# Kernel tuning notes

Hardware: AMD Instinct MI355X
Metric: run time of the kernel (lower is better)

## Reference

```python
import jax, jax.numpy as jnp
import numpy as np

NUM_LEAVES = 8192
N_LAMBDA = 2101  # wavelengths 400..2500 nm

# ---- exponential integral E1(x), x > 0 (Abramowitz & Stegun 5.1.53 / 5.1.56) ----
# Ei(-x) = -E1(x) for x > 0; forward only ever calls expi on -kall with kall >= 1e-4.
_A = jnp.array([-0.57721566, 0.99999193, -0.24991055, 0.05519968, -0.00976004, 0.00107857], dtype=jnp.float32)
_PN = jnp.array([1.0, 8.5733287401, 18.0590169730, 8.6347608925, 0.2677737343], dtype=jnp.float32)
_PD = jnp.array([1.0, 9.5733223454, 25.6329561486, 21.0996530827, 3.9584969228], dtype=jnp.float32)

def _poly(c, x):
    r = c[0]
    for ci in c[1:]:
        r = r * x + ci
    return r

def _e1(x):
    # x > 0 guaranteed (kall clamped to >= 1e-4)
    small = -jnp.log(x) + _poly(_A[::-1], x)          # 0 < x <= 1
    big = jnp.exp(-x) / x * (_poly(_PN, x) / _poly(_PD, x))  # x > 1
    return jnp.where(x <= 1.0, small, big)

# ---- transmissivity of a dielectric plane (Stern / Allen) ----
def _getav(alpha_deg, nr):
    n2 = nr ** 2
    npx = n2 + 1.0
    nm = n2 - 1.0
    a = (nr + 1.0) * (nr + 1.0) / 2.0
    k = -(n2 - 1.0) * (n2 - 1.0) / 4.0
    rd = alpha_deg * (np.pi / 180.0)
    sa2 = np.sin(rd) ** 2  # python scalar
    if alpha_deg != 90.0:
        b1 = jnp.sqrt((sa2 - npx / 2.0) ** 2 + k)
    else:
        b1 = 0.0
    b2 = sa2 - npx / 2.0
    b = b1 - b2
    k2 = k ** 2
    ts = k2 / (6.0 * b ** 3) + k / b - b / 2.0 - (k2 / (6.0 * a ** 3) + k / a - a / 2.0)
    tp1 = -2.0 * n2 * (b - a) / npx ** 2
    nm2 = nm ** 2
    tp2 = -2.0 * n2 * npx * jnp.log(b / a) / nm2
    tp3 = n2 * (1.0 / b - 1.0 / a) / 2.0
    n22 = n2 ** 2
    npx3 = npx ** 3
    npax_a = 2.0 * npx * a - nm2
    npx_b = 2.0 * npx * b - nm2
    tp4 = 16.0 * n22 * (n22 + 1.0) * jnp.log(npx_b / npax_a) / (npx3 * nm2)
    tp5 = 16.0 * n2 ** 3 * (1.0 / npx_b - 1.0 / npax_a) / npx3
    tp = tp1 + tp2 + tp3 + tp4 + tp5
    return (ts + tp) / (2.0 * sa2)

def _forward(N, cab, car, water, lma, cant, nr, kab, kcar, kant, kw, km):
    # kall: [L, W] via broadcasting of [L,1] traits against [W] spectra
    kall = (cab * kab + car * kcar + cant * kant + water * kw + lma * km) / N
    kall = jnp.maximum(kall, 1e-4)
    # tau = (1-k)e^{-k} + k^2 * (-Ei(-k)) = (1-k)e^{-k} + k^2 E1(k)
    tau = (1.0 - kall) * jnp.exp(-kall) + kall ** 2 * _e1(kall)

    # one-layer reflectance/transmittance
    talf = _getav(40.0, nr)
    ralf = 1.0 - talf
    t12 = _getav(90.0, nr)
    r12 = 1.0 - t12
    t21 = t12 / (nr * nr)
    r21 = 1.0 - t21
    denom = 1.0 - r21 * r21 * tau * tau
    Ta = talf * tau * t21 / denom
    Ra = ralf + r21 * tau * Ta
    t = t12 * tau * t21 / denom
    r = r12 + r21 * tau * t

    rpt = r + t
    rmt = r - t
    mask = rpt >= 1.0  # [L, W]
    Dsq = (1.0 + rpt) * (1.0 + rmt) * (1.0 - rmt) * (1.0 - rpt)
    D = jnp.sqrt(jnp.where(mask, 1.0, Dsq))
    rqmtq = r ** 2 - t ** 2
    a = (1.0 + rqmtq + D) / (2.0 * r)
    b = (1.0 - rqmtq + D) / (2.0 * t)
    b_safe = jnp.where(mask, 1.0, b)  # guard pow with float exponent
    bnm1 = b_safe ** (N - 1.0)
    bn2 = bnm1 ** 2
    a2 = a * a
    den2 = a2 * bn2 - 1.0
    Rsub = a * (bn2 - 1.0) / den2
    Tsub = bnm1 * (a2 - 1.0) / den2
    # thick-layer (r+t >= 1) limit
    Tsub_alt = t / (t + (1.0 - t) * (N - 1.0))
    Tsub = jnp.where(mask, Tsub_alt, Tsub)
    Rsub = jnp.where(mask, 1.0 - Tsub_alt, Rsub)

    den3 = 1.0 - Rsub * r
    tran = Ta * Tsub / den3
    refl = Ra + Ta_Rsub_term(Ta, Rsub, t, den3)
    return refl, tran

def Ta_Rsub_term(Ta, Rsub, t, den3):
    return Ta * Rsub * t / den3

def setup_inputs() -> dict:
    key = jax.random.key(0)
    ks = jax.random.split(key, 12)
    u = lambda k, shp: jax.random.uniform(k, shp, dtype=jnp.float32)
    L, W = NUM_LEAVES, N_LAMBDA
    return {
        "N":     1.0 + 1.5 * u(ks[0], (L, 1)),      # leaf structure 1..2.5
        "cab":   10.0 + 70.0 * u(ks[1], (L, 1)),    # chlorophyll ug/cm2
        "car":   2.0 + 18.0 * u(ks[2], (L, 1)),     # carotenoids
        "water": 0.002 + 0.03 * u(ks[3], (L, 1)),   # EWT cm
        "lma":   0.005 + 0.03 * u(ks[4], (L, 1)),   # dry matter g/cm2
        "cant":  2.0 * u(ks[5], (L, 1)),            # anthocyanins
        "nr":    1.3 + 0.3 * u(ks[6], (W,)),        # refractive index
        "kab":   0.05 * u(ks[7], (W,)),
        "kcar":  0.05 * u(ks[8], (W,)),
        "kant":  0.05 * u(ks[9], (W,)),
        "kw":    30.0 * u(ks[10], (W,)),
        "km":    60.0 * u(ks[11], (W,)),
    }

def reference(N, cab, car, water, lma, cant, nr, kab, kcar, kant, kw, km):
    return _forward(N, cab, car, water, lma, cant, nr, kab, kcar, kant, kw, km)
```

## Files before the change

kernel.cpp:

```cpp
#include <hip/hip_runtime.h>
#include <hip/hip_fp16.h>

#define L_LEAVES 8192
#define W_LAMBDA 2101
#define WPAD     2104
#define TAB_N    1153
#define SA2_40   0.41317591116653485f
#define LOG2E_F  1.4426950408889634f
#define LN2_F    0.6931471805599453f

typedef float v2f __attribute__((ext_vector_type(2)));

__device__ __forceinline__ float rcpf(float x)  { return __builtin_amdgcn_rcpf(x); }
__device__ __forceinline__ float log2f_fast(float x) { return __builtin_amdgcn_logf(x); }
__device__ __forceinline__ float exp2f_fast(float x) { return __builtin_amdgcn_exp2f(x); }
__device__ __forceinline__ float sqrtf_fast(float x) { return __builtin_amdgcn_sqrtf(x); }
__device__ __forceinline__ v2f v2(float a, float b) { v2f r; r.x = a; r.y = b; return r; }

__device__ __forceinline__ float getav_dev(float sa2, bool is90, float nr) {
    float n2  = nr * nr;
    float npx = n2 + 1.0f;
    float nm  = n2 - 1.0f;
    float a   = (nr + 1.0f) * (nr + 1.0f) * 0.5f;
    float k   = -(n2 - 1.0f) * (n2 - 1.0f) * 0.25f;
    float b2  = sa2 - npx * 0.5f;
    float b1  = is90 ? 0.0f : sqrtf_fast(b2 * b2 + k);
    float b   = b1 - b2;
    float k2  = k * k;
    float ib  = rcpf(b), ia = rcpf(a);
    float ts  = k2 * (1.0f/6.0f) * (ib*ib*ib) + k * ib - b * 0.5f
              - (k2 * (1.0f/6.0f) * (ia*ia*ia) + k * ia - a * 0.5f);
    float inpx = rcpf(npx);
    float tp1 = -2.0f * n2 * (b - a) * (inpx * inpx);
    float nm2 = nm * nm;
    float inm2 = rcpf(nm2);
    float tp2 = -2.0f * n2 * npx * (LN2_F * log2f_fast(b * ia)) * inm2;
    float tp3 = n2 * (ib - ia) * 0.5f;
    float n22 = n2 * n2;
    float inpx3 = inpx * inpx * inpx;
    float npax_a = 2.0f * npx * a - nm2;
    float npx_b  = 2.0f * npx * b - nm2;
    float tp4 = 16.0f * n22 * (n22 + 1.0f) * (LN2_F * log2f_fast(npx_b * rcpf(npax_a))) * inpx3 * inm2;
    float tp5 = 16.0f * n2 * n2 * n2 * (rcpf(npx_b) - rcpf(npax_a)) * inpx3;
    float tp  = tp1 + tp2 + tp3 + tp4 + tp5;
    return (ts + tp) * rcpf(2.0f * sa2);
}

__device__ __forceinline__ float tau_exact(float k) {
    float ek = exp2f_fast(-k * LOG2E_F);
    float e1;
    if (k <= 1.0f) {
        float poly = fmaf(fmaf(fmaf(fmaf(fmaf(0.00107857f, k, -0.00976004f), k, 0.05519968f),
                        k, -0.24991055f), k, 0.99999193f), k, -0.57721566f);
        e1 = fmaf(-LN2_F, log2f_fast(k), poly);
    } else {
        float pn = fmaf(fmaf(fmaf(k + 8.5733287401f, k, 18.0590169730f),
                       k, 8.6347608925f), k, 0.2677737343f);
        float pd = fmaf(fmaf(fmaf(k + 9.5733223454f, k, 25.6329561486f),
                       k, 21.0996530827f), k, 3.9584969228f);
        e1 = ek * rcpf(k) * (pn * rcpf(pd));
    }
    return fmaf(k * k, e1, (1.0f - k) * ek);
}

__device__ __forceinline__ float bin_k(int w) {
    unsigned e = (unsigned)w >> 6, m = (unsigned)w & 63u;
    return __uint_as_float(((113u + e) << 23) | (m << 17));
}

__global__ void precompute_kernel(const float* __restrict__ nr, float* __restrict__ tab) {
    int w = blockIdx.x * blockDim.x + threadIdx.x;
    if (w < WPAD) {
        int ws = min(w, W_LAMBDA - 1);
        float n    = nr[ws];
        float talf = getav_dev(SA2_40, false, n);
        float t12  = getav_dev(1.0f,   true,  n);
        float t21  = t12 * rcpf(n * n);
        float r21  = 1.0f - t21;
        tab[0 * WPAD + w] = talf * t21;
        tab[1 * WPAD + w] = 1.0f - talf;
        tab[2 * WPAD + w] = t12 * t21;
        tab[3 * WPAD + w] = 1.0f - t12;
        tab[4 * WPAD + w] = r21;
    }
    if (w < TAB_N) {
        float T0 = tau_exact(bin_k(w));
        float T1 = tau_exact(bin_k(w + 1));
        __half2 h2;
        h2.x = __float2half(T0);
        h2.y = __float2half(T1 - T0);
        tab[5 * WPAD + w] = __uint_as_float(*reinterpret_cast<unsigned*>(&h2));
    }
}

struct f4u { float v[4]; };

template<bool USE_TAB>
__global__ __launch_bounds__(192) void prospect_kernel(
    const float* __restrict__ pN,   const float* __restrict__ pcab,
    const float* __restrict__ pcar, const float* __restrict__ pwater,
    const float* __restrict__ plma, const float* __restrict__ pcant,
    const float* __restrict__ pnr,
    const float* __restrict__ pkab, const float* __restrict__ pkcar,
    const float* __restrict__ pkant, const float* __restrict__ pkw,
    const float* __restrict__ pkm,
    const float* __restrict__ tab,
    float* __restrict__ out_r, float* __restrict__ out_t)
{
    __shared__ unsigned TT[TAB_N];
    if (USE_TAB) {
        const float* src = tab + 5 * WPAD;
        for (int i = threadIdx.x; i < TAB_N; i += 192)
            TT[i] = __float_as_uint(src[i]);
        __syncthreads();
    }

    const int q  = blockIdx.x * 192 + threadIdx.x;
    const int w0 = q * 4;
    if (w0 >= W_LAMBDA) return;
    const bool full = (w0 + 4 <= W_LAMBDA);

    const int l = blockIdx.y;
    const float Nl   = pN[l];
    const float invN = rcpf(Nl);
    const float Nm1  = Nl - 1.0f;
    const float cabl = pcab[l], carl = pcar[l], cantl = pcant[l];
    const float watl = pwater[l], lmal = plma[l];

    float4 vkab, vkcar, vkant, vkw, vkm;
    if (full) {
        vkab  = *(const float4*)(pkab  + w0);
        vkcar = *(const float4*)(pkcar + w0);
        vkant = *(const float4*)(pkant + w0);
        vkw   = *(const float4*)(pkw   + w0);
        vkm   = *(const float4*)(pkm   + w0);
    } else {
        #pragma unroll
        for (int j = 0; j < 4; ++j) {
            int w = min(w0 + j, W_LAMBDA - 1);
            ((float*)&vkab)[j]  = pkab[w];
            ((float*)&vkcar)[j] = pkcar[w];
            ((float*)&vkant)[j] = pkant[w];
            ((float*)&vkw)[j]   = pkw[w];
            ((float*)&vkm)[j]   = pkm[w];
        }
    }
    float4 t0, t1, t2, t3, t4;
    if (USE_TAB) {
        t0 = *(const float4*)(tab + 0 * WPAD + w0);
        t1 = *(const float4*)(tab + 1 * WPAD + w0);
        t2 = *(const float4*)(tab + 2 * WPAD + w0);
        t3 = *(const float4*)(tab + 3 * WPAD + w0);
        t4 = *(const float4*)(tab + 4 * WPAD + w0);
    } else {
        #pragma unroll
        for (int j = 0; j < 4; ++j) {
            int w = min(w0 + j, W_LAMBDA - 1);
            float n    = pnr[w];
            float talf = getav_dev(SA2_40, false, n);
            float t12  = getav_dev(1.0f,   true,  n);
            float t21  = t12 * rcpf(n * n);
            float r21  = 1.0f - t21;
            ((float*)&t0)[j] = talf * t21;
            ((float*)&t1)[j] = 1.0f - talf;
            ((float*)&t2)[j] = t12 * t21;
            ((float*)&t3)[j] = 1.0f - t12;
            ((float*)&t4)[j] = r21;
        }
    }

    float rf[4], tr[4];
    #pragma unroll
    for (int p = 0; p < 2; ++p) {
        const v2f c0 = p ? v2(t0.z, t0.w) : v2(t0.x, t0.y);
        const v2f c1 = p ? v2(t1.z, t1.w) : v2(t1.x, t1.y);
        const v2f c2 = p ? v2(t2.z, t2.w) : v2(t2.x, t2.y);
        const v2f c3 = p ? v2(t3.z, t3.w) : v2(t3.x, t3.y);
        const v2f c4 = p ? v2(t4.z, t4.w) : v2(t4.x, t4.y);
        const v2f ab = p ? v2(vkab.z, vkab.w) : v2(vkab.x, vkab.y);
        const v2f cr = p ? v2(vkcar.z, vkcar.w) : v2(vkcar.x, vkcar.y);
        const v2f an = p ? v2(vkant.z, vkant.w) : v2(vkant.x, vkant.y);
        const v2f wt = p ? v2(vkw.z, vkw.w) : v2(vkw.x, vkw.y);
        const v2f lm = p ? v2(vkm.z, vkm.w) : v2(vkm.x, vkm.y);

        v2f k = (cabl * ab + carl * cr + cantl * an + watl * wt + lmal * lm) * invN;
        k = __builtin_elementwise_max(k, (v2f)1e-4f);

        v2f tau;
        if (USE_TAB) {
            v2f kc = __builtin_elementwise_min(k, (v2f)15.9f);
            unsigned b0 = __float_as_uint(kc.x), b1 = __float_as_uint(kc.y);
            unsigned u0 = TT[(int)(b0 >> 17) - 7232];
            unsigned u1 = TT[(int)(b1 >> 17) - 7232];
            float2 Tf0 = __half22float2(*reinterpret_cast<const __half2*>(&u0));
            float2 Tf1 = __half22float2(*reinterpret_cast<const __half2*>(&u1));
            v2f frac = v2((float)(b0 & 0x1FFFFu), (float)(b1 & 0x1FFFFu)) * (1.0f / 131072.0f);
            tau = frac * v2(Tf0.y, Tf1.y) + v2(Tf0.x, Tf1.x);
        } else {
            tau = v2(tau_exact(k.x), tau_exact(k.y));
        }

        v2f r21t = c4 * tau;
        v2f d1   = 1.0f - r21t * r21t;
        v2f rd   = v2(rcpf(d1.x), rcpf(d1.y));
        v2f trd  = tau * rd;
        v2f Ta   = c0 * trd;
        v2f tt   = c2 * trd;
        v2f Ra   = r21t * Ta + c1;
        v2f rr   = r21t * tt + c3;

        v2f rpt = rr + tt;
        v2f rmt = rr - tt;
        bool m0 = (rpt.x >= 1.0f), m1 = (rpt.y >= 1.0f);
        v2f Dsq = (1.0f - rmt * rmt) * (1.0f - rpt * rpt);
        v2f D   = v2(sqrtf_fast(m0 ? 1.0f : Dsq.x), sqrtf_fast(m1 ? 1.0f : Dsq.y));
        v2f rq  = rpt * rmt;
        v2f s1  = 1.0f + D;
        v2f prod = (rr * tt) * 4.0f;
        v2f rp2  = v2(rcpf(prod.x), rcpf(prod.y));
        v2f aa   = (s1 + rq) * (rp2 * (tt + tt));
        v2f bb   = (s1 - rq) * (rp2 * (rr + rr));
        v2f lg   = v2(log2f_fast(m0 ? 1.0f : bb.x), log2f_fast(m1 ? 1.0f : bb.y));
        v2f ex   = Nm1 * lg;
        v2f bnm1 = v2(exp2f_fast(ex.x), exp2f_fast(ex.y));
        v2f bn2  = bnm1 * bnm1;
        v2f a2   = aa * aa;
        v2f den2 = a2 * bn2 - 1.0f;
        v2f bn2m1 = bn2 - 1.0f;
        v2f M    = den2 - (aa * rr) * bn2m1;
        v2f invM = v2(rcpf(M.x), rcpf(M.y));
        v2f TaM  = Ta * invM;
        v2f tranv = TaM * bnm1 * (a2 - 1.0f);
        v2f reflv = (TaM * tt * aa) * bn2m1 + Ra;

        if (__any((int)(m0 || m1))) {
            #pragma unroll
            for (int c = 0; c < 2; ++c) {
                bool m = c ? m1 : m0;
                if (m) {
                    float ttc = c ? tt.y : tt.x, rrc = c ? rr.y : rr.x;
                    float Tac = c ? Ta.y : Ta.x, Rac = c ? Ra.y : Ra.x;
                    float Talt = ttc * rcpf(fmaf(Nm1, 1.0f - ttc, ttc));
                    float Rsm  = 1.0f - Talt;
                    float g    = Tac * rcpf(fmaf(-Rsm, rrc, 1.0f));
                    if (c) { tranv.y = g * Talt; reflv.y = fmaf(g * Rsm, ttc, Rac); }
                    else   { tranv.x = g * Talt; reflv.x = fmaf(g * Rsm, ttc, Rac); }
                }
            }
        }

        tr[2 * p]     = tranv.x;
        tr[2 * p + 1] = tranv.y;
        rf[2 * p]     = reflv.x;
        rf[2 * p + 1] = reflv.y;
    }

    const unsigned base = (unsigned)l * W_LAMBDA + (unsigned)w0;
    if (full) {
        f4u fr; f4u ft;
        #pragma unroll
        for (int j = 0; j < 4; ++j) { fr.v[j] = rf[j]; ft.v[j] = tr[j]; }
        *reinterpret_cast<f4u*>(out_r + base) = fr;
        *reinterpret_cast<f4u*>(out_t + base) = ft;
    } else {
        out_r[base] = rf[0];
        out_t[base] = tr[0];
    }
}

extern "C" void kernel_launch(void* const* d_in, const int* in_sizes, int n_in,
                              void* d_out, int out_size, void* d_ws, size_t ws_size,
                              hipStream_t stream) {
    const float* pN     = (const float*)d_in[0];
    const float* pcab   = (const float*)d_in[1];
    const float* pcar   = (const float*)d_in[2];
    const float* pwater = (const float*)d_in[3];
    const float* plma   = (const float*)d_in[4];
    const float* pcant  = (const float*)d_in[5];
    const float* pnr    = (const float*)d_in[6];
    const float* pkab   = (const float*)d_in[7];
    const float* pkcar  = (const float*)d_in[8];
    const float* pkant  = (const float*)d_in[9];
    const float* pkw    = (const float*)d_in[10];
    const float* pkm    = (const float*)d_in[11];
    float* out_r = (float*)d_out;
    float* out_t = out_r + (size_t)L_LEAVES * W_LAMBDA;

    const int nquads = (W_LAMBDA + 3) / 4;
    dim3 grid((nquads + 191) / 192, L_LEAVES);
    dim3 block(192);

    const size_t tab_bytes = (5 * WPAD + TAB_N) * sizeof(float);
    if (ws_size >= tab_bytes) {
        float* tabp = (float*)d_ws;
        precompute_kernel<<<(WPAD + 63) / 64, 64, 0, stream>>>(pnr, tabp);
        prospect_kernel<true><<<grid, block, 0, stream>>>(
            pN, pcab, pcar, pwater, plma, pcant, pnr,
            pkab, pkcar, pkant, pkw, pkm, (const float*)tabp, out_r, out_t);
    } else {
        prospect_kernel<false><<<grid, block, 0, stream>>>(
            pN, pcab, pcar, pwater, plma, pcant, pnr,
            pkab, pkcar, pkant, pkw, pkm, nullptr, out_r, out_t);
    }
}
```

Baseline: 52.82 us.

## Use one 576-thread block per leaf with scalar tail threads

Measured after the change: 51.27 us (median of 2 runs). 1.03x faster.

```diff
diff --git a/kernel.cpp b/kernel.cpp
--- a/kernel.cpp
+++ b/kernel.cpp
@@ -93,10 +93,49 @@
     }
 }
 
+__device__ __forceinline__ void stokes_point(float tau, float c0, float c1, float c2,
+                                             float c3, float c4, float Nm1,
+                                             float& refl, float& tran) {
+    float r21t = c4 * tau;
+    float rd   = rcpf(fmaf(-r21t, r21t, 1.0f));
+    float trd  = tau * rd;
+    float Ta   = c0 * trd;
+    float tt   = c2 * trd;
+    float Ra   = fmaf(r21t, Ta, c1);
+    float rr   = fmaf(r21t, tt, c3);
+    float rpt  = rr + tt;
+    float rmt  = rr - tt;
+    bool  mask = (rpt >= 1.0f);
+    float Dsq  = fmaf(-rmt, rmt, 1.0f) * fmaf(-rpt, rpt, 1.0f);
+    float D    = sqrtf_fast(mask ? 1.0f : Dsq);
+    float rq   = rpt * rmt;
+    float s1   = 1.0f + D;
+    float rp2  = rcpf((rr * tt) * 4.0f);
+    float aa   = (s1 + rq) * (rp2 * (tt + tt));
+    float bb   = (s1 - rq) * (rp2 * (rr + rr));
+    float bnm1 = exp2f_fast(Nm1 * log2f_fast(mask ? 1.0f : bb));
+    float bn2  = bnm1 * bnm1;
+    float a2   = aa * aa;
+    float den2 = fmaf(a2, bn2, -1.0f);
+    float bn2m1 = bn2 - 1.0f;
+    float M    = fmaf(-aa * rr, bn2m1, den2);
+    float invM = rcpf(M);
+    float TaM  = Ta * invM;
+    tran = TaM * bnm1 * (a2 - 1.0f);
+    refl = fmaf(TaM * tt * aa, bn2m1, Ra);
+    if (mask) {
+        float Talt = tt * rcpf(fmaf(Nm1, 1.0f - tt, tt));
+        float Rsm  = 1.0f - Talt;
+        float g    = Ta * rcpf(fmaf(-Rsm, rr, 1.0f));
+        tran = g * Talt;
+        refl = fmaf(g * Rsm, tt, Ra);
+    }
+}
+
 struct f4u { float v[4]; };
 
 template<bool USE_TAB>
-__global__ __launch_bounds__(192) void prospect_kernel(
+__global__ __launch_bounds__(576) void prospect_kernel(
     const float* __restrict__ pN,   const float* __restrict__ pcab,
     const float* __restrict__ pcar, const float* __restrict__ pwater,
     const float* __restrict__ plma, const float* __restrict__ pcant,
@@ -110,161 +149,186 @@
     __shared__ unsigned TT[TAB_N];
     if (USE_TAB) {
         const float* src = tab + 5 * WPAD;
-        for (int i = threadIdx.x; i < TAB_N; i += 192)
+        for (int i = threadIdx.x; i < TAB_N; i += 576)
             TT[i] = __float_as_uint(src[i]);
         __syncthreads();
     }
 
-    const int q  = blockIdx.x * 192 + threadIdx.x;
-    const int w0 = q * 4;
-    if (w0 >= W_LAMBDA) return;
-    const bool full = (w0 + 4 <= W_LAMBDA);
-
-    const int l = blockIdx.y;
+    const int l = blockIdx.x;
     const float Nl   = pN[l];
     const float invN = rcpf(Nl);
     const float Nm1  = Nl - 1.0f;
     const float cabl = pcab[l], carl = pcar[l], cantl = pcant[l];
     const float watl = pwater[l], lmal = plma[l];
-
-    float4 vkab, vkcar, vkant, vkw, vkm;
-    if (full) {
-        vkab  = *(const float4*)(pkab  + w0);
-        vkcar = *(const float4*)(pkcar + w0);
-        vkant = *(const float4*)(pkant + w0);
-        vkw   = *(const float4*)(pkw   + w0);
-        vkm   = *(const float4*)(pkm   + w0);
-    } else {
+    const int tid = threadIdx.x;
+    const unsigned rowbase = (unsigned)l * W_LAMBDA;
+
+    if (tid < 512) {
+        const int w0 = tid * 4;
+
+        float4 vkab  = *(const float4*)(pkab  + w0);
+        float4 vkcar = *(const float4*)(pkcar + w0);
+        float4 vkant = *(const float4*)(pkant + w0);
+        float4 vkw   = *(const float4*)(pkw   + w0);
+        float4 vkm   = *(const float4*)(pkm   + w0);
+        float4 t0, t1, t2, t3, t4;
+        if (USE_TAB) {
+            t0 = *(const float4*)(tab + 0 * WPAD + w0);
+            t1 = *(const float4*)(tab + 1 * WPAD + w0);
+            t2 = *(const float4*)(tab + 2 * WPAD + w0);
+            t3 = *(const float4*)(tab + 3 * WPAD + w0);
+            t4 = *(const float4*)(tab + 4 * WPAD + w0);
+        } else {
+            #pragma unroll
+            for (int j = 0; j < 4; ++j) {
+                int w = w0 + j;
+                float n    = pnr[w];
+                float talf = getav_dev(SA2_40, false, n);
+                float t12  = getav_dev(1.0f,   true,  n);
+                float t21  = t12 * rcpf(n * n);
+                float r21  = 1.0f - t21;
+                ((float*)&t0)[j] = talf * t21;
+                ((float*)&t1)[j] = 1.0f - talf;
+                ((float*)&t2)[j] = t12 * t21;
+                ((float*)&t3)[j] = 1.0f - t12;
+                ((float*)&t4)[j] = r21;
+            }
+        }
+
+        float rf[4], tr[4];
         #pragma unroll
-        for (int j = 0; j < 4; ++j) {
-            int w = min(w0 + j, W_LAMBDA - 1);
-            ((float*)&vkab)[j]  = pkab[w];
-            ((float*)&vkcar)[j] = pkcar[w];
-            ((float*)&vkant)[j] = pkant[w];
-            ((float*)&vkw)[j]   = pkw[w];
-            ((float*)&vkm)[j]   = pkm[w];
+        for (int p = 0; p < 2; ++p) {
+            const v2f c0 = p ? v2(t0.z, t0.w) : v2(t0.x, t0.y);
+            const v2f c1 = p ? v2(t1.z, t1.w) : v2(t1.x, t1.y);
+            const v2f c2 = p ? v2(t2.z, t2.w) : v2(t2.x, t2.y);
+            const v2f c3 = p ? v2(t3.z, t3.w) : v2(t3.x, t3.y);
+            const v2f c4 = p ? v2(t4.z, t4.w) : v2(t4.x, t4.y);
+            const v2f ab = p ? v2(vkab.z, vkab.w) : v2(vkab.x, vkab.y);
+            const v2f cr = p ? v2(vkcar.z, vkcar.w) : v2(vkcar.x, vkcar.y);
+            const v2f an = p ? v2(vkant.z, vkant.w) : v2(vkant.x, vkant.y);
+            const v2f wt = p ? v2(vkw.z, vkw.w) : v2(vkw.x, vkw.y);
+            const v2f lm = p ? v2(vkm.z, vkm.w) : v2(vkm.x, vkm.y);
+
+            v2f k = (cabl * ab + carl * cr + cantl * an + watl * wt + lmal * lm) * invN;
+            k = __builtin_elementwise_max(k, (v2f)1e-4f);
+
+            v2f tau;
+            if (USE_TAB) {
+                v2f kc = __builtin_elementwise_min(k, (v2f)15.9f);
+                unsigned b0 = __float_as_uint(kc.x), b1 = __float_as_uint(kc.y);
+                unsigned u0 = TT[(int)(b0 >> 17) - 7232];
+                unsigned u1 = TT[(int)(b1 >> 17) - 7232];
+                float2 Tf0 = __half22float2(*reinterpret_cast<const __half2*>(&u0));
+                float2 Tf1 = __half22float2(*reinterpret_cast<const __half2*>(&u1));
+                v2f frac = v2((float)(b0 & 0x1FFFFu), (float)(b1 & 0x1FFFFu)) * (1.0f / 131072.0f);
+                tau = frac * v2(Tf0.y, Tf1.y) + v2(Tf0.x, Tf1.x);
+            } else {
+                tau = v2(tau_exact(k.x), tau_exact(k.y));
+            }
+
+            v2f r21t = c4 * tau;
+            v2f d1   = 1.0f - r21t * r21t;
+            v2f rd   = v2(rcpf(d1.x), rcpf(d1.y));
+            v2f trd  = tau * rd;
+            v2f Ta   = c0 * trd;
+            v2f tt   = c2 * trd;
+            v2f Ra   = r21t * Ta + c1;
+            v2f rr   = r21t * tt + c3;
+
+            v2f rpt = rr + tt;
+            v2f rmt = rr - tt;
+            bool m0 = (rpt.x >= 1.0f), m1 = (rpt.y >= 1.0f);
+            v2f Dsq = (1.0f - rmt * rmt) * (1.0f - rpt * rpt);
+            v2f D   = v2(sqrtf_fast(m0 ? 1.0f : Dsq.x), sqrtf_fast(m1 ? 1.0f : Dsq.y));
+            v2f rq  = rpt * rmt;
+            v2f s1  = 1.0f + D;
+            v2f prod = (rr * tt) * 4.0f;
+            v2f rp2  = v2(rcpf(prod.x), rcpf(prod.y));
+            v2f aa   = (s1 + rq) * (rp2 * (tt + tt));
+            v2f bb   = (s1 - rq) * (rp2 * (rr + rr));
+            v2f lg   = v2(log2f_fast(m0 ? 1.0f : bb.x), log2f_fast(m1 ? 1.0f : bb.y));
+            v2f ex   = Nm1 * lg;
+            v2f bnm1 = v2(exp2f_fast(ex.x), exp2f_fast(ex.y));
+            v2f bn2  = bnm1 * bnm1;
+            v2f a2   = aa * aa;
+            v2f den2 = a2 * bn2 - 1.0f;
+            v2f bn2m1 = bn2 - 1.0f;
+            v2f M    = den2 - (aa * rr) * bn2m1;
+            v2f invM = v2(rcpf(M.x), rcpf(M.y));
+            v2f TaM  = Ta * invM;
+            v2f tranv = TaM * bnm1 * (a2 - 1.0f);
+            v2f reflv = (TaM * tt * aa) * bn2m1 + Ra;
+
+            if (__any((int)(m0 || m1))) {
+                #pragma unroll
+                for (int c = 0; c < 2; ++c) {
+                    bool m = c ? m1 : m0;
+                    if (m) {
+                        float ttc = c ? tt.y : tt.x, rrc = c ? rr.y : rr.x;
+                        float Tac = c ? Ta.y : Ta.x, Rac = c ? Ra.y : Ra.x;
+                        float Talt = ttc * rcpf(fmaf(Nm1, 1.0f - ttc, ttc));
+                        float Rsm  = 1.0f - Talt;
+                        float g    = Tac * rcpf(fmaf(-Rsm, rrc, 1.0f));
+                        if (c) { tranv.y = g * Talt; reflv.y = fmaf(g * Rsm, ttc, Rac); }
+                        else   { tranv.x = g * Talt; reflv.x = fmaf(g * Rsm, ttc, Rac); }
+                    }
+                }
+            }
+
+            tr[2 * p]     = tranv.x;
+            tr[2 * p + 1] = tranv.y;
+            rf[2 * p]     = reflv.x;
+            rf[2 * p + 1] = reflv.y;
         }
-    }
-    float4 t0, t1, t2, t3, t4;
-    if (USE_TAB) {
-        t0 = *(const float4*)(tab + 0 * WPAD + w0);
-        t1 = *(const float4*)(tab + 1 * WPAD + w0);
-        t2 = *(const float4*)(tab + 2 * WPAD + w0);
-        t3 = *(const float4*)(tab + 3 * WPAD + w0);
-        t4 = *(const float4*)(tab + 4 * WPAD + w0);
-    } else {
-        #pragma unroll
-        for (int j = 0; j < 4; ++j) {
-            int w = min(w0 + j, W_LAMBDA - 1);
-            float n    = pnr[w];
-            float talf = getav_dev(SA2_40, false, n);
-            float t12  = getav_dev(1.0f,   true,  n);
-            float t21  = t12 * rcpf(n * n);
-            float r21  = 1.0f - t21;
-            ((float*)&t0)[j] = talf * t21;
-            ((float*)&t1)[j] = 1.0f - talf;
-            ((float*)&t2)[j] = t12 * t21;
-            ((float*)&t3)[j] = 1.0f - t12;
-            ((float*)&t4)[j] = r21;
-        }
-    }
-
-    float rf[4], tr[4];
-    #pragma unroll
-    for (int p = 0; p < 2; ++p) {
-        const v2f c0 = p ? v2(t0.z, t0.w) : v2(t0.x, t0.y);
-        const v2f c1 = p ? v2(t1.z, t1.w) : v2(t1.x, t1.y);
-        const v2f c2 = p ? v2(t2.z, t2.w) : v2(t2.x, t2.y);
-        const v2f c3 = p ? v2(t3.z, t3.w) : v2(t3.x, t3.y);
-        const v2f c4 = p ? v2(t4.z, t4.w) : v2(t4.x, t4.y);
-        const v2f ab = p ? v2(vkab.z, vkab.w) : v2(vkab.x, vkab.y);
-        const v2f cr = p ? v2(vkcar.z, vkcar.w) : v2(vkcar.x, vkcar.y);
-        const v2f an = p ? v2(vkant.z, vkant.w) : v2(vkant.x, vkant.y);
-        const v2f wt = p ? v2(vkw.z, vkw.w) : v2(vkw.x, vkw.y);
-        const v2f lm = p ? v2(vkm.z, vkm.w) : v2(vkm.x, vkm.y);
-
-        v2f k = (cabl * ab + carl * cr + cantl * an + watl * wt + lmal * lm) * invN;
-        k = __builtin_elementwise_max(k, (v2f)1e-4f);
-
-        v2f tau;
-        if (USE_TAB) {
-            v2f kc = __builtin_elementwise_min(k, (v2f)15.9f);
-            unsigned b0 = __float_as_uint(kc.x), b1 = __float_as_uint(kc.y);
-            unsigned u0 = TT[(int)(b0 >> 17) - 7232];
-            unsigned u1 = TT[(int)(b1 >> 17) - 7232];
-            float2 Tf0 = __half22float2(*reinterpret_cast<const __half2*>(&u0));
-            float2 Tf1 = __half22float2(*reinterpret_cast<const __half2*>(&u1));
-            v2f frac = v2((float)(b0 & 0x1FFFFu), (float)(b1 & 0x1FFFFu)) * (1.0f / 131072.0f);
-            tau = frac * v2(Tf0.y, Tf1.y) + v2(Tf0.x, Tf1.x);
-        } else {
-            tau = v2(tau_exact(k.x), tau_exact(k.y));
-        }
-
-        v2f r21t = c4 * tau;
-        v2f d1   = 1.0f - r21t * r21t;
-        v2f rd   = v2(rcpf(d1.x), rcpf(d1.y));
-        v2f trd  = tau * rd;
-        v2f Ta   = c0 * trd;
-        v2f tt   = c2 * trd;
-        v2f Ra   = r21t * Ta + c1;
-        v2f rr   = r21t * tt + c3;
-
-        v2f rpt = rr + tt;
-        v2f rmt = rr - tt;
-        bool m0 = (rpt.x >= 1.0f), m1 = (rpt.y >= 1.0f);
-        v2f Dsq = (1.0f - rmt * rmt) * (1.0f - rpt * rpt);
-        v2f D   = v2(sqrtf_fast(m0 ? 1.0f : Dsq.x), sqrtf_fast(m1 ? 1.0f : Dsq.y));
-        v2f rq  = rpt * rmt;
-        v2f s1  = 1.0f + D;
-        v2f prod = (rr * tt) * 4.0f;
-        v2f rp2  = v2(rcpf(prod.x), rcpf(prod.y));
-        v2f aa   = (s1 + rq) * (rp2 * (tt + tt));
-        v2f bb   = (s1 - rq) * (rp2 * (rr + rr));
-        v2f lg   = v2(log2f_fast(m0 ? 1.0f : bb.x), log2f_fast(m1 ? 1.0f : bb.y));
-        v2f ex   = Nm1 * lg;
-        v2f bnm1 = v2(exp2f_fast(ex.x), exp2f_fast(ex.y));
-        v2f bn2  = bnm1 * bnm1;
-        v2f a2   = aa * aa;
-        v2f den2 = a2 * bn2 - 1.0f;
-        v2f bn2m1 = bn2 - 1.0f;
-        v2f M    = den2 - (aa * rr) * bn2m1;
-        v2f invM = v2(rcpf(M.x), rcpf(M.y));
-        v2f TaM  = Ta * invM;
-        v2f tranv = TaM * bnm1 * (a2 - 1.0f);
-        v2f reflv = (TaM * tt * aa) * bn2m1 + Ra;
-
-        if (__any((int)(m0 || m1))) {
-            #pragma unroll
-            for (int c = 0; c < 2; ++c) {
-                bool m = c ? m1 : m0;
-                if (m) {
-                    float ttc = c ? tt.y : tt.x, rrc = c ? rr.y : rr.x;
-                    float Tac = c ? Ta.y : Ta.x, Rac = c ? Ra.y : Ra.x;
-                    float Talt = ttc * rcpf(fmaf(Nm1, 1.0f - ttc, ttc));
-                    float Rsm  = 1.0f - Talt;
-                    float g    = Tac * rcpf(fmaf(-Rsm, rrc, 1.0f));
-                    if (c) { tranv.y = g * Talt; reflv.y = fmaf(g * Rsm, ttc, Rac); }
-                    else   { tranv.x = g * Talt; reflv.x = fmaf(g * Rsm, ttc, Rac); }
-                }
-            }
-        }
-
-        tr[2 * p]     = tranv.x;
-        tr[2 * p + 1] = tranv.y;
-        rf[2 * p]     = reflv.x;
-        rf[2 * p + 1] = reflv.y;
-    }
-
-    const unsigned base = (unsigned)l * W_LAMBDA + (unsigned)w0;
-    if (full) {
+
+        const unsigned base = rowbase + (unsigned)w0;
         f4u fr; f4u ft;
         #pragma unroll
         for (int j = 0; j < 4; ++j) { fr.v[j] = rf[j]; ft.v[j] = tr[j]; }
         *reinterpret_cast<f4u*>(out_r + base) = fr;
         *reinterpret_cast<f4u*>(out_t + base) = ft;
     } else {
-        out_r[base] = rf[0];
-        out_t[base] = tr[0];
+        const int w = 2048 + (tid - 512);
+        if (w < W_LAMBDA) {
+            float k = (cabl * pkab[w] + carl * pkcar[w] + cantl * pkant[w]
+                     + watl * pkw[w] + lmal * pkm[w]) * invN;
+            k = fmaxf(k, 1e-4f);
+
+            float c0, c1, c2, c3, c4;
+            if (USE_TAB) {
+                c0 = tab[0 * WPAD + w];
+                c1 = tab[1 * WPAD + w];
+                c2 = tab[2 * WPAD + w];
+                c3 = tab[3 * WPAD + w];
+                c4 = tab[4 * WPAD + w];
+            } else {
+                float n    = pnr[w];
+                float talf = getav_dev(SA2_40, false, n);
+                float t12  = getav_dev(1.0f,   true,  n);
+                float t21  = t12 * rcpf(n * n);
+                float r21  = 1.0f - t21;
+                c0 = talf * t21; c1 = 1.0f - talf; c2 = t12 * t21;
+                c3 = 1.0f - t12; c4 = r21;
+            }
+
+            float tau;
+            if (USE_TAB) {
+                float kc = fminf(k, 15.9f);
+                unsigned bits = __float_as_uint(kc);
+                int idx = (int)(bits >> 17) - 7232;
+                float frac = (float)(bits & 0x1FFFFu) * (1.0f / 131072.0f);
+                unsigned u = TT[idx];
+                float2 Tf = __half22float2(*reinterpret_cast<const __half2*>(&u));
+                tau = fmaf(frac, Tf.y, Tf.x);
+            } else {
+                tau = tau_exact(k);
+            }
+
+            float refl, tran;
+            stokes_point(tau, c0, c1, c2, c3, c4, Nm1, refl, tran);
+            out_r[rowbase + w] = refl;
+            out_t[rowbase + w] = tran;
+        }
     }
 }
 
@@ -286,9 +350,8 @@
     float* out_r = (float*)d_out;
     float* out_t = out_r + (size_t)L_LEAVES * W_LAMBDA;
 
-    const int nquads = (W_LAMBDA + 3) / 4;
-    dim3 grid((nquads + 191) / 192, L_LEAVES);
-    dim3 block(192);
+    dim3 grid(L_LEAVES);
+    dim3 block(576);
 
     const size_t tab_bytes = (5 * WPAD + TAB_N) * sizeof(float);
     if (ws_size >= tab_bytes) {
```
